# Kernel optimization log

Hardware: AMD Instinct MI355X
Metric: run time of the kernel (lower is better)

## Reference

```python
import jax, jax.numpy as jnp
import numpy as np

N_NODES = 10000
N_EDGES = 256000
H = 128   # n_hidden_feats
P = 64    # n_product_feats
NB = 8    # n_basis
NS = 10   # n_species
RH = 64   # radial MLP hidden width
RC = 5.0  # r_cutoff
AVG = 25.6  # avg_n_neighbors


def _radial(r):
    # Bessel radial basis * polynomial cutoff envelope (p = n_polynomial_cutoff = 5). r: [E,1]
    n = jnp.arange(1, NB + 1, dtype=r.dtype)
    bessel = jnp.sqrt(2.0 / RC) * jnp.sin(n * jnp.pi * r / RC) / r  # [E,NB]
    u = r / RC
    p = 5.0
    env = 1.0 - 0.5 * (p + 1) * (p + 2) * u**p + p * (p + 2) * u**(p + 1) - 0.5 * p * (p + 1) * u**(p + 2)
    env = jnp.where(u < 1.0, env, 0.0)
    return bessel * env


def _mlp(x, Ws):
    for W in Ws[:-1]:
        x = jax.nn.silu(x @ W)
    return x @ Ws[-1]


def _B0(w, A0, A1):
    # correlation-3 symmetric contractions to a scalar target; w: [N,5,P]
    dot = jnp.sum(A1 * A1, axis=-1)  # [N,P]  (rank-1 . rank-1)
    return (w[:, 0] * A0 + w[:, 1] * A0**2 + w[:, 2] * A0**3
            + w[:, 3] * dot + w[:, 4] * A0 * dot)


def _forward(positions, shifts, node_attrs,
             W_embed, Wsc1, Wup0_1, R1_0, R1_1, R1_2, R1_3,
             Wout0_1, Wout1_1, Wp0_1, Wp1_1, Wl0_1, Wl1_1,
             Wsc2, Wup0_2, Wup1_2, R2_0, R2_1, R2_2, R2_3,
             Wout0_2, Wout1_2, Wp0_2, Wl0_2,
             idx_i, idx_j):
    v = positions[idx_i] - positions[idx_j] - shifts                    # [E,3]
    r = jnp.maximum(jnp.linalg.norm(v, axis=-1, keepdims=True), 1e-9)   # [E,1]
    Y1 = v / r                                                          # Cartesian harmonics, l=1
    edge_feats = _radial(r)                                             # [E,NB]

    feats0 = node_attrs @ W_embed                                       # [N,H] scalar node embedding

    # ---- interaction 1: node feats l=0, edge attrs l<=1 -> targets l<=1 ----
    sc0 = jnp.einsum('nk,kch,nc->nh', node_attrs, Wsc1, feats0)         # per-species residual
    h0 = feats0 @ Wup0_1
    w = _mlp(edge_feats, (R1_0, R1_1, R1_2, R1_3)).reshape(-1, 2, H)    # tp weights per edge
    h0j = h0[idx_j]                                                     # [E,H]
    m0 = w[:, 0] * h0j                                                  # 0x0->0
    m1 = (w[:, 1] * h0j)[:, :, None] * Y1[:, None, :]                   # 0x1->1, [E,H,3]
    a0 = jax.ops.segment_sum(m0, idx_i, num_segments=N_NODES) / AVG
    a1 = jax.ops.segment_sum(m1, idx_i, num_segments=N_NODES) / AVG
    A0 = a0 @ Wout0_1                                                   # [N,P]
    A1 = jnp.einsum('nhd,hp->npd', a1, Wout1_1)                         # [N,P,3]

    # ---- product basis 1 (correlation 3, targets l=0 and l=1) ----
    wp0 = jnp.einsum('nk,kqp->nqp', node_attrs, Wp0_1)                  # [N,5,P]
    wp1 = jnp.einsum('nk,kqp->nqp', node_attrs, Wp1_1)                  # [N,4,P]
    B0 = _B0(wp0, A0, A1)
    dot = jnp.sum(A1 * A1, axis=-1)
    B1 = (wp1[:, 0] + wp1[:, 1] * A0 + wp1[:, 2] * A0**2 + wp1[:, 3] * dot)[:, :, None] * A1
    out0 = B0 @ Wl0_1 + sc0                                             # [N,H]
    out1 = jnp.einsum('npd,ph->nhd', B1, Wl1_1)                         # [N,H,3] (sc has no l=1 part)

    # ---- interaction 2: node feats l<=1, targets l<=1; product target l=0 ----
    sc0b = jnp.einsum('nk,kch,nc->nh', node_attrs, Wsc2, out0)
    g0 = out0 @ Wup0_2
    g1 = jnp.einsum('nhd,hg->ngd', out1, Wup1_2)
    w2 = _mlp(edge_feats, (R2_0, R2_1, R2_2, R2_3)).reshape(-1, 5, H)   # 5 tp paths
    g0j = g0[idx_j]
    g1j = g1[idx_j]
    Y1e = Y1[:, None, :]
    m0 = w2[:, 0] * g0j + w2[:, 3] * jnp.sum(g1j * Y1e, axis=-1)        # 0x0->0, 1x1->0 (dot)
    m1 = ((w2[:, 1] * g0j)[:, :, None] * Y1e                             # 0x1->1
          + w2[:, 2][:, :, None] * g1j                                   # 1x0->1
          + w2[:, 4][:, :, None] * jnp.cross(g1j, jnp.broadcast_to(Y1e, g1j.shape)))  # 1x1->1
    a0 = jax.ops.segment_sum(m0, idx_i, num_segments=N_NODES) / AVG
    a1 = jax.ops.segment_sum(m1, idx_i, num_segments=N_NODES) / AVG
    A0 = a0 @ Wout0_2
    A1 = jnp.einsum('nhd,hp->npd', a1, Wout1_2)
    wp0 = jnp.einsum('nk,kqp->nqp', node_attrs, Wp0_2)
    out0b = _B0(wp0, A0, A1) @ Wl0_2 + sc0b                             # [N,H]

    # torch returns [feats[:, :H] per layer]; the first H flattened columns are the scalar block
    return jnp.stack([out0, out0b], axis=0)                             # [2,N,H]


def setup_inputs() -> dict:
    key = jax.random.key(0)
    ks = iter(jax.random.split(key, 40))

    def nrm(shape, fan_in):
        return jax.random.normal(next(ks), shape, dtype=jnp.float32) / np.sqrt(fan_in)

    positions = jax.random.normal(next(ks), (N_NODES, 3), dtype=jnp.float32) * 8.0
    idx_i = jax.random.randint(next(ks), (N_EDGES,), 0, N_NODES)
    idx_j = jax.random.randint(next(ks), (N_EDGES,), 0, N_NODES)
    shifts = jnp.zeros((N_EDGES, 3), jnp.float32)
    species = jax.random.randint(next(ks), (N_NODES,), 0, NS)
    node_attrs = jax.nn.one_hot(species, NS, dtype=jnp.float32)

    return dict(
        positions=positions, shifts=shifts, node_attrs=node_attrs,
        W_embed=nrm((NS, H), NS),
        Wsc1=nrm((NS, H, H), H), Wup0_1=nrm((H, H), H),
        R1_0=nrm((NB, RH), NB), R1_1=nrm((RH, RH), RH), R1_2=nrm((RH, RH), RH), R1_3=nrm((RH, 2 * H), RH),
        Wout0_1=nrm((H, P), H), Wout1_1=nrm((H, P), H),
        Wp0_1=nrm((NS, 5, P), 1.0), Wp1_1=nrm((NS, 4, P), 1.0),
        Wl0_1=nrm((P, H), P), Wl1_1=nrm((P, H), P),
        Wsc2=nrm((NS, H, H), H), Wup0_2=nrm((H, H), H), Wup1_2=nrm((H, H), H),
        R2_0=nrm((NB, RH), NB), R2_1=nrm((RH, RH), RH), R2_2=nrm((RH, RH), RH), R2_3=nrm((RH, 5 * H), RH),
        Wout0_2=nrm((H, P), H), Wout1_2=nrm((H, P), H),
        Wp0_2=nrm((NS, 5, P), 1.0),
        Wl0_2=nrm((P, H), P),
        idx_i=idx_i, idx_j=idx_j,
    )


def reference(positions, shifts, node_attrs,
              W_embed, Wsc1, Wup0_1, R1_0, R1_1, R1_2, R1_3,
              Wout0_1, Wout1_1, Wp0_1, Wp1_1, Wl0_1, Wl1_1,
              Wsc2, Wup0_2, Wup1_2, R2_0, R2_1, R2_2, R2_3,
              Wout0_2, Wout1_2, Wp0_2, Wl0_2,
              idx_i, idx_j):
    return _forward(positions, shifts, node_attrs,
                    W_embed, Wsc1, Wup0_1, R1_0, R1_1, R1_2, R1_3,
                    Wout0_1, Wout1_1, Wp0_1, Wp1_1, Wl0_1, Wl1_1,
                    Wsc2, Wup0_2, Wup1_2, R2_0, R2_1, R2_2, R2_3,
                    Wout0_2, Wout1_2, Wp0_2, Wl0_2,
                    idx_i, idx_j)
```

## Files before the change

### kernel.cpp

```cpp
#include <hip/hip_runtime.h>
#include <math.h>

#define NN 10000
#define NE 256000
#define HD 128
#define PD 64
#define NBASIS 8
#define NSPEC 10
#define RHID 64
#define RCUT 5.0f
#define INV_AVG 0.0390625f
#define PI_F 3.14159265358979f
#define ECAP 12288
#define NACTCAP 8192
#define RSZ 819

__device__ __forceinline__ float silu(float x) {
    return x / (1.0f + expf(-x));
}

__global__ __launch_bounds__(256) void k_initTables(
    const float* __restrict__ na_, const float* __restrict__ We,
    const float* __restrict__ Wsc1, const float* __restrict__ Wup01,
    const float* __restrict__ Wup02, const float* __restrict__ Wsc2,
    int* __restrict__ spec, int* __restrict__ ecnt, int* cnt, int* eTot,
    int* __restrict__ scurG, int* __restrict__ actLst,
    float* __restrict__ sc0s, float* __restrict__ h0s,
    float* __restrict__ g0d, float* __restrict__ sc0bd) {
    __shared__ float ls[HD];
    int b = blockIdx.x;
    if (b < 40) {
        int n = b * 256 + threadIdx.x;
        if (n == 0) { *cnt = 0; *eTot = 0; }
        if (n < NSPEC) scurG[n] = 0;
        if (n < NACTCAP) actLst[n] = -1;
        if (n >= NN) return;
        ecnt[n] = 0;
        int s = 0;
        for (int k = 0; k < NSPEC; k++)
            if (na_[n * NSPEC + k] > 0.5f) s = k;
        spec[n] = s;
    } else {
        int s = b - 40;
        int t = threadIdx.x;
        if (t < HD) {
            float acc1 = 0.f, acc2 = 0.f;
            for (int c = 0; c < HD; c++) {
                float fe = We[s * HD + c];
                acc1 += fe * Wsc1[((size_t)s * HD + c) * HD + t];
                acc2 += fe * Wup01[c * HD + t];
            }
            sc0s[s * HD + t] = acc1;
            h0s[s * HD + t] = acc2;
            ls[t] = acc1;
        }
        __syncthreads();
        if (t < HD) {
            float a1 = 0.f, a2 = 0.f;
            for (int c = 0; c < HD; c++) {
                float v = ls[c];
                a1 += v * Wup02[c * HD + t];
                a2 += v * Wsc2[((size_t)s * HD + c) * HD + t];
            }
            g0d[s * HD + t] = a1;
            sc0bd[s * HD + t] = a2;
        }
    }
}

__global__ __launch_bounds__(256) void k_compact(
    const float* __restrict__ pos, const float* __restrict__ shifts,
    const int* __restrict__ ii, const int* __restrict__ jj,
    int* cnt, int* __restrict__ ecnt,
    int* __restrict__ ui, int* __restrict__ uj,
    float* __restrict__ uY, float* __restrict__ uF) {
    __shared__ int lTot;
    __shared__ int blockBase;
    int t = threadIdx.x;
    if (t == 0) lTot = 0;
    __syncthreads();
    int e0 = (blockIdx.x * 256 + t) * 4;
    int iv[4], jv[4], keep[4];
    float vx[4], vy[4], vz[4], rr[4];
    #pragma unroll
    for (int k = 0; k < 4; k++) {
        int e = e0 + k;
        int i = ii[e], j = jj[e];
        iv[k] = i; jv[k] = j;
        float x = pos[i * 3 + 0] - pos[j * 3 + 0] - shifts[e * 3 + 0];
        float y = pos[i * 3 + 1] - pos[j * 3 + 1] - shifts[e * 3 + 1];
        float z = pos[i * 3 + 2] - pos[j * 3 + 2] - shifts[e * 3 + 2];
        float r = sqrtf(x * x + y * y + z * z);
        r = fmaxf(r, 1e-9f);
        vx[k] = x; vy[k] = y; vz[k] = z; rr[k] = r;
        keep[k] = (r < RCUT) ? 1 : 0;
    }
    int myCnt = keep[0] + keep[1] + keep[2] + keep[3];
    int myOff = 0;
    if (myCnt) myOff = atomicAdd(&lTot, myCnt);
    __syncthreads();
    if (t == 0) blockBase = atomicAdd(cnt, lTot);
    __syncthreads();
    int slot = blockBase + myOff;
    #pragma unroll
    for (int k = 0; k < 4; k++) {
        if (!keep[k]) continue;
        int i = iv[k];
        atomicAdd(&ecnt[i], 1);
        ui[slot] = i; uj[slot] = jv[k];
        float r = rr[k];
        float inv = 1.0f / r;
        uY[slot * 3 + 0] = vx[k] * inv;
        uY[slot * 3 + 1] = vy[k] * inv;
        uY[slot * 3 + 2] = vz[k] * inv;
        float u = r * (1.0f / RCUT);
        float u5 = u * u * u * u * u;
        float env = 1.0f - 21.0f * u5 + 35.0f * u5 * u - 15.0f * u5 * u * u;
        float c0 = 0.6324555320336759f * env * inv;
        float th = PI_F * u;
        float s1, c1;
        __sincosf(th, &s1, &c1);
        float two_c1 = 2.0f * c1;
        float sp = 0.f, sn = s1;
        uF[slot * NBASIS + 0] = c0 * sn;
        #pragma unroll
        for (int b = 1; b < NBASIS; b++) {
            float s_new = two_c1 * sn - sp;
            sp = sn; sn = s_new;
            uF[slot * NBASIS + b] = c0 * sn;
        }
        slot++;
    }
}

__global__ __launch_bounds__(256) void k_assignPlace(
    const int* __restrict__ ecnt, const int* __restrict__ spec,
    int* __restrict__ ebase, int* __restrict__ ecur,
    int* eTot, int* scurG,
    int* __restrict__ actIndex, int* __restrict__ actList) {
    __shared__ int lTot;
    __shared__ int blockBase;
    __shared__ int lHist[NSPEC];
    __shared__ int lBase[NSPEC];
    int t = threadIdx.x;
    int n = blockIdx.x * 256 + t;
    if (t == 0) lTot = 0;
    if (t < NSPEC) lHist[t] = 0;
    __syncthreads();
    int ec = (n < NN) ? ecnt[n] : 0;
    int s = (n < NN) ? spec[n] : 0;
    bool act = (ec > 0);
    int myOff = 0, myIdx = 0;
    if (act) {
        myOff = atomicAdd(&lTot, ec);
        myIdx = atomicAdd(&lHist[s], 1);
    }
    __syncthreads();
    if (t == 0) blockBase = atomicAdd(eTot, lTot);
    if (t < NSPEC) lBase[t] = (lHist[t] > 0) ? atomicAdd(&scurG[t], lHist[t]) : 0;
    __syncthreads();
    if (n < NN) {
        if (act) {
            int b = blockBase + myOff;
            ebase[n] = b;
            ecur[n] = b;
            int rank = lBase[s] + myIdx;
            if (rank < RSZ) {
                int p = s * RSZ + rank;
                actList[p] = n;
                actIndex[n] = p;
            } else {
                actIndex[n] = -1;
            }
        } else {
            actIndex[n] = -1;
        }
    }
}

__global__ __launch_bounds__(256) void k_sortFill(
    const int* cnt, const int* __restrict__ ui, const int* __restrict__ uj,
    const float* __restrict__ uY, const float* __restrict__ uF,
    int* __restrict__ ecur, int* __restrict__ sj,
    float* __restrict__ sY, float* __restrict__ sF,
    const int* __restrict__ spec, const float* __restrict__ sc0s,
    const float* __restrict__ sc0bd,
    float* __restrict__ out0g, float* __restrict__ outbg) {
    int b = blockIdx.x;
    if (b < 48) {
        int e = b * 256 + threadIdx.x;
        int n = *cnt; if (n > ECAP) n = ECAP;
        if (e >= n) return;
        int slot = atomicAdd(&ecur[ui[e]], 1);
        if (slot >= ECAP) return;
        sj[slot] = uj[e];
        #pragma unroll
        for (int d = 0; d < 3; d++) sY[slot * 3 + d] = uY[e * 3 + d];
        #pragma unroll
        for (int bb = 0; bb < NBASIS; bb++) sF[slot * NBASIS + bb] = uF[e * NBASIS + bb];
    } else {
        int t = (b - 48) * 256 + threadIdx.x;
        int n = t >> 6, c = t & 63;
        if (n >= NN) return;
        int s = spec[n];
        out0g[(size_t)n * HD + c] = sc0s[s * HD + c];
        out0g[(size_t)n * HD + 64 + c] = sc0s[s * HD + 64 + c];
        outbg[(size_t)n * HD + c] = sc0bd[s * HD + c];
        outbg[(size_t)n * HD + 64 + c] = sc0bd[s * HD + 64 + c];
    }
}

__global__ __launch_bounds__(256) void k_hid(
    const int* cnt, const float* __restrict__ sF,
    const float* __restrict__ A0, const float* __restrict__ A1, const float* __restrict__ A2,
    const float* __restrict__ B0, const float* __restrict__ B1, const float* __restrict__ B2,
    float* __restrict__ xh1, float* __restrict__ xh2) {
    __shared__ float sf[64 * 9];
    __shared__ float xA[64 * 65];
    __shared__ float xB[64 * 65];
    int t = threadIdx.x;
    int ne = *cnt; if (ne > ECAP) ne = ECAP;
    int eBase = blockIdx.x * 64;
    if (eBase >= ne) return;
    const float* W0 = (blockIdx.y == 0) ? A0 : B0;
    const float* W1 = (blockIdx.y == 0) ? A1 : B1;
    const float* W2 = (blockIdx.y == 0) ? A2 : B2;
    float* dst = (blockIdx.y == 0) ? xh1 : xh2;
    if (t < 128) {
        float4 v = *(const float4*)(sF + (size_t)eBase * NBASIS + t * 4);
        int e = t >> 1, c = (t & 1) * 4;
        float* d = &sf[e * 9 + c];
        d[0] = v.x; d[1] = v.y; d[2] = v.z; d[3] = v.w;
    }
    __syncthreads();
    int sgrp = t >> 4;
    int cg = (t & 15) * 4;
    {
        float acc[4][4] = {};
        #pragma unroll
        for (int c = 0; c < NBASIS; c++) {
            float xk[4];
            #pragma unroll
            for (int k = 0; k < 4; k++) xk[k] = sf[(sgrp * 4 + k) * 9 + c];
            float4 wv = *(const float4*)(W0 + c * RHID + cg);
            float wq[4] = {wv.x, wv.y, wv.z, wv.w};
            #pragma unroll
            for (int k = 0; k < 4; k++)
                #pragma unroll
                for (int q = 0; q < 4; q++)
                    acc[k][q] += xk[k] * wq[q];
        }
        #pragma unroll
        for (int k = 0; k < 4; k++)
            #pragma unroll
            for (int q = 0; q < 4; q++)
                xA[(sgrp * 4 + k) * 65 + cg + q] = silu(acc[k][q]);
    }
    __syncthreads();
    {
        float acc[4][4] = {};
        for (int c = 0; c < RHID; c++) {
            float xk[4];
            #pragma unroll
            for (int k = 0; k < 4; k++) xk[k] = xA[(sgrp * 4 + k) * 65 + c];
            float4 wv = *(const float4*)(W1 + c * RHID + cg);
            float wq[4] = {wv.x, wv.y, wv.z, wv.w};
            #pragma unroll
            for (int k = 0; k < 4; k++)
                #pragma unroll
                for (int q = 0; q < 4; q++)
                    acc[k][q] += xk[k] * wq[q];
        }
        #pragma unroll
        for (int k = 0; k < 4; k++)
            #pragma unroll
            for (int q = 0; q < 4; q++)
                xB[(sgrp * 4 + k) * 65 + cg + q] = silu(acc[k][q]);
    }
    __syncthreads();
    {
        float acc[4][4] = {};
        for (int c = 0; c < RHID; c++) {
            float xk[4];
            #pragma unroll
            for (int k = 0; k < 4; k++) xk[k] = xB[(sgrp * 4 + k) * 65 + c];
            float4 wv = *(const float4*)(W2 + c * RHID + cg);
            float wq[4] = {wv.x, wv.y, wv.z, wv.w};
            #pragma unroll
            for (int k = 0; k < 4; k++)
                #pragma unroll
                for (int q = 0; q < 4; q++)
                    acc[k][q] += xk[k] * wq[q];
        }
        #pragma unroll
        for (int k = 0; k < 4; k++) {
            int e = eBase + sgrp * 4 + k;
            if (e < ne) {
                *(float4*)(dst + (size_t)e * RHID + cg) =
                    make_float4(silu(acc[k][0]), silu(acc[k][1]),
                                silu(acc[k][2]), silu(acc[k][3]));
            }
        }
    }
}

__global__ __launch_bounds__(256) void k_wmat(
    const int* cnt, const float* __restrict__ xh1, const float* __restrict__ xh2,
    const float* __restrict__ A3, const float* __restrict__ B3,
    float* __restrict__ ew1, float* __restrict__ ew2) {
    __shared__ float sX[64 * 65];
    int t = threadIdx.x;
    int ne = *cnt; if (ne > ECAP) ne = ECAP;
    int y = blockIdx.y;
    int eBase = blockIdx.x * 64;
    if (eBase >= ne) return;
    const float* X; const float* W; float* dst; int ncol, col0;
    if (y < 2) { X = xh1; W = A3; dst = ew1; ncol = 2 * HD; col0 = y * 128; }
    else       { X = xh2; W = B3; dst = ew2; ncol = 5 * HD; col0 = (y - 2) * 128; }
    {
        const float4* src = (const float4*)(X + (size_t)eBase * RHID);
        #pragma unroll
        for (int it = 0; it < 4; it++) {
            int idx = t + it * 256;
            float4 v = src[idx];
            int e = idx >> 4, c4 = (idx & 15) * 4;
            float* d = &sX[e * 65 + c4];
            d[0] = v.x; d[1] = v.y; d[2] = v.z; d[3] = v.w;
        }
    }
    __syncthreads();
    int sgrp = t >> 4;
    int cg = col0 + (t & 15) * 8;
    float acc[4][8] = {};
    for (int c = 0; c < RHID; c++) {
        float xk[4];
        #pragma unroll
        for (int k = 0; k < 4; k++) xk[k] = sX[(sgrp * 4 + k) * 65 + c];
        float4 wA = *(const float4*)(W + (size_t)c * ncol + cg);
        float4 wB = *(const float4*)(W + (size_t)c * ncol + cg + 4);
        float wv[8] = {wA.x, wA.y, wA.z, wA.w, wB.x, wB.y, wB.z, wB.w};
        #pragma unroll
        for (int k = 0; k < 4; k++)
            #pragma unroll
            for (int q = 0; q < 8; q++)
                acc[k][q] += xk[k] * wv[q];
    }
    #pragma unroll
    for (int k = 0; k < 4; k++) {
        int e = eBase + sgrp * 4 + k;
        *(float4*)(dst + (size_t)e * ncol + cg) =
            make_float4(acc[k][0], acc[k][1], acc[k][2], acc[k][3]);
        *(float4*)(dst + (size_t)e * ncol + cg + 4) =
            make_float4(acc[k][4], acc[k][5], acc[k][6], acc[k][7]);
    }
}

__global__ __launch_bounds__(256) void k_agg1(
    const int* __restrict__ actList,
    const int* __restrict__ ebase, const int* __restrict__ ecnt,
    const int* __restrict__ sj, const float* __restrict__ sY,
    const float* __restrict__ ew, const int* __restrict__ spec,
    const float* __restrict__ h0s, float* __restrict__ a0c, float* __restrict__ a1c) {
    int lane = threadIdx.x & 63;
    int ia = (blockIdx.x * 256 + threadIdx.x) >> 6;
    int h = blockIdx.y * 64;
    int n = actList[ia];
    if (n < 0) return;
    int eb = ebase[n], ec = ecnt[n];
    float a0 = 0.f;
    float a1[3] = {0,0,0};
    for (int idx = eb; idx < eb + ec; idx++) {
        int j = sj[idx];
        int sp = spec[j];
        float h0 = h0s[sp * HD + h + lane];
        const float* w = ew + (size_t)idx * 256;
        float w0 = w[h + lane], w1 = w[128 + h + lane];
        a0 += w0 * h0;
        float m1 = w1 * h0;
        #pragma unroll
        for (int d = 0; d < 3; d++) a1[d] += m1 * sY[idx * 3 + d];
    }
    a0c[(size_t)ia * HD + h + lane] = a0 * INV_AVG;
    #pragma unroll
    for (int d = 0; d < 3; d++)
        a1c[((size_t)d * NACTCAP + ia) * HD + h + lane] = a1[d] * INV_AVG;
}

__global__ __launch_bounds__(256) void k_proj(
    const int* __restrict__ actList,
    const float* __restrict__ x0buf, const float* __restrict__ x1buf,
    const float* __restrict__ W0, const float* __restrict__ W1,
    float* __restrict__ am0, float* __restrict__ am1) {
    __shared__ float sX[16 * HD];
    int lane = threadIdx.x & 63;
    int w = __builtin_amdgcn_readfirstlane((int)(threadIdx.x >> 6));
    int y = blockIdx.y;
    const float* X = (y == 0) ? x0buf : (x1buf + (size_t)(y - 1) * NACTCAP * HD);
    const float* W = (y == 0) ? W0 : W1;
    int iaBase = blockIdx.x * 16;
    {
        const float4* src = (const float4*)(X + (size_t)iaBase * HD);
        float4* d4 = (float4*)sX;
        #pragma unroll
        for (int it = 0; it < 2; it++)
            d4[threadIdx.x + it * 256] = src[threadIdx.x + it * 256];
    }
    __syncthreads();
    bool any = false;
    int ia0 = iaBase + w * 4;
    #pragma unroll
    for (int k = 0; k < 4; k++) any = any || (actList[ia0 + k] >= 0);
    if (!any) return;
    float* dst = (y == 0) ? am0 : (am1 + (size_t)(y - 1) * NACTCAP * PD);
    int w4 = w * 4;
    float acc[4] = {0,0,0,0};
    for (int c = 0; c < HD; c += 4) {
        float4 xv[4];
        #pragma unroll
        for (int k = 0; k < 4; k++) xv[k] = *(const float4*)&sX[(w4 + k) * HD + c];
        #pragma unroll
        for (int cc = 0; cc < 4; cc++) {
            float wv = W[(c + cc) * PD + lane];
            #pragma unroll
            for (int k = 0; k < 4; k++) {
                float xc = (cc==0)?xv[k].x:(cc==1)?xv[k].y:(cc==2)?xv[k].z:xv[k].w;
                acc[k] += xc * wv;
            }
        }
    }
    #pragma unroll
    for (int k = 0; k < 4; k++) dst[(size_t)(ia0 + k) * PD + lane] = acc[k];
}

__global__ __launch_bounds__(256) void k_bout(
    const int* __restrict__ actList,
    const float* __restrict__ am0, const float* __restrict__ am1,
    const int* __restrict__ spec,
    const float* __restrict__ Wp0, const float* __restrict__ Wp1,
    const float* __restrict__ Wl0, const float* __restrict__ Wl1,
    const float* __restrict__ sc0s,
    float* __restrict__ out0g, float* __restrict__ out0c, float* __restrict__ out1c) {
    __shared__ float sB[4][8][PD];
    int lane = threadIdx.x & 63;
    int w = __builtin_amdgcn_readfirstlane((int)(threadIdx.x >> 6));
    int y = blockIdx.y;
    int bs = y >> 1, h = (y & 1) * 64;
    int ia0 = (blockIdx.x * 4 + w) * 8;
    int nv[8], sk[8];
    bool any = false;
    #pragma unroll
    for (int k = 0; k < 8; k++) {
        nv[k] = actList[ia0 + k];
        any = any || (nv[k] >= 0);
        sk[k] = spec[(nv[k] >= 0) ? nv[k] : 0];
    }
    if (!any) return;
    #pragma unroll
    for (int k = 0; k < 8; k++) {
        int ia = ia0 + k;
        int s = sk[k];
        float A0v = am0[(size_t)ia * PD + lane];
        float a1x = am1[((size_t)0 * NACTCAP + ia) * PD + lane];
        float a1y = am1[((size_t)1 * NACTCAP + ia) * PD + lane];
        float a1z = am1[((size_t)2 * NACTCAP + ia) * PD + lane];
        float dot = a1x * a1x + a1y * a1y + a1z * a1z;
        float A02 = A0v * A0v;
        float B;
        if (bs == 0) {
            const float* wp = Wp0 + (size_t)(s * 5) * PD;
            B = wp[lane] * A0v + wp[PD + lane] * A02 + wp[2 * PD + lane] * A02 * A0v +
                wp[3 * PD + lane] * dot + wp[4 * PD + lane] * A0v * dot;
        } else {
            const float* wp = Wp1 + (size_t)(s * 4) * PD;
            float fac = wp[lane] + wp[PD + lane] * A0v + wp[2 * PD + lane] * A02 + wp[3 * PD + lane] * dot;
            float a1d = (bs == 1) ? a1x : ((bs == 2) ? a1y : a1z);
            B = fac * a1d;
        }
        sB[w][k][lane] = B;
    }
    const float* Wl = (bs == 0) ? Wl0 : Wl1;
    float o[8] = {0,0,0,0,0,0,0,0};
    for (int q = 0; q < PD; q += 4) {
        float4 bq[8];
        #pragma unroll
        for (int k = 0; k < 8; k++) bq[k] = *(const float4*)&sB[w][k][q];
        #pragma unroll
        for (int qq = 0; qq < 4; qq++) {
            float wl = Wl[(q + qq) * HD + h + lane];
            #pragma unroll
            for (int k = 0; k < 8; k++) {
                float b = (qq==0)?bq[k].x:(qq==1)?bq[k].y:(qq==2)?bq[k].z:bq[k].w;
                o[k] += b * wl;
            }
        }
    }
    if (bs == 0) {
        #pragma unroll
        for (int k = 0; k < 8; k++) {
            int ia = ia0 + k;
            float v = o[k] + sc0s[sk[k] * HD + h + lane];
            if (nv[k] >= 0) out0g[(size_t)nv[k] * HD + h + lane] = v;
            out0c[(size_t)ia * HD + h + lane] = v;
        }
    } else {
        float* dst = out1c + (size_t)(bs - 1) * NACTCAP * HD;
        #pragma unroll
        for (int k = 0; k < 8; k++)
            dst[(size_t)(ia0 + k) * HD + h + lane] = o[k];
    }
}

__global__ __launch_bounds__(256) void k_g(
    const int* __restrict__ actList, const int* __restrict__ spec,
    const float* __restrict__ out0c, const float* __restrict__ out1c,
    const float* __restrict__ Wsc2, const float* __restrict__ Wup02, const float* __restrict__ Wup12,
    float* __restrict__ sc0bc, float* __restrict__ g0c, float* __restrict__ g1c) {
    __shared__ float sX[64 * 129];
    __shared__ int sSpec[64];
    __shared__ int sB0, sAny, sMis;
    int t = threadIdx.x;
    int st = blockIdx.y;
    int slotBase = blockIdx.x * 64;
    const float* X = (st <= 1) ? out0c : (out1c + (size_t)(st - 2) * NACTCAP * HD);
    if (t < 64) {
        int n = actList[slotBase + t];
        sSpec[t] = (n >= 0) ? spec[n] : -1;
    }
    __syncthreads();
    if (t == 0) {
        int sb = 0, any = 0, mis = 0;
        for (int k = 0; k < 64; k++) {
            int sv = sSpec[k];
            if (sv >= 0) {
                if (!any) { sb = sv; any = 1; }
                else if (sv != sb) mis = 1;
            }
        }
        sB0 = sb; sAny = any; sMis = mis;
    }
    __syncthreads();
    if (!sAny) return;
    {
        const float4* src = (const float4*)(X + (size_t)slotBase * HD);
        #pragma unroll
        for (int it = 0; it < 8; it++) {
            int idx = t + it * 256;
            float4 v = src[idx];
            int e = idx >> 5, c4 = (idx & 31) * 4;
            float* d = &sX[e * 129 + c4];
            d[0] = v.x; d[1] = v.y; d[2] = v.z; d[3] = v.w;
        }
    }
    __syncthreads();
    const float* Wt = (st == 0) ? (Wsc2 + (size_t)sB0 * HD * HD)
                    : ((st == 1) ? Wup02 : Wup12);
    float* dst = (st == 0) ? sc0bc : ((st == 1) ? g0c : (g1c + (size_t)(st - 2) * NACTCAP * HD));
    int sgrp = t >> 4;
    int cg = (t & 15) * 8;
    float acc[4][8] = {};
    for (int c = 0; c < HD; c++) {
        float xk[4];
        #pragma unroll
        for (int k = 0; k < 4; k++) xk[k] = sX[(sgrp * 4 + k) * 129 + c];
        float4 wA = *(const float4*)(Wt + (size_t)c * HD + cg);
        float4 wB = *(const float4*)(Wt + (size_t)c * HD + cg + 4);
        float wv[8] = {wA.x, wA.y, wA.z, wA.w, wB.x, wB.y, wB.z, wB.w};
        #pragma unroll
        for (int k = 0; k < 4; k++)
            #pragma unroll
            for (int q = 0; q < 8; q++)
                acc[k][q] += xk[k] * wv[q];
    }
    #pragma unroll
    for (int k = 0; k < 4; k++) {
        int slot = slotBase + sgrp * 4 + k;
        *(float4*)(dst + (size_t)slot * HD + cg) =
            make_float4(acc[k][0], acc[k][1], acc[k][2], acc[k][3]);
        *(float4*)(dst + (size_t)slot * HD + cg + 4) =
            make_float4(acc[k][4], acc[k][5], acc[k][6], acc[k][7]);
    }
    if (st == 0 && sMis) {
        __syncthreads();
        for (int k = 0; k < 64; k++) {
            int sv = sSpec[k];
            if (sv < 0 || sv == sB0) continue;
            if (t < HD) {
                const float* Wm = Wsc2 + (size_t)sv * HD * HD;
                float p = 0.f;
                for (int c = 0; c < HD; c++) p += sX[k * 129 + c] * Wm[c * HD + t];
                sc0bc[(size_t)(slotBase + k) * HD + t] = p;
            }
        }
    }
}

__global__ __launch_bounds__(256) void k_agg2(
    const int* __restrict__ actList,
    const int* __restrict__ ebase, const int* __restrict__ ecnt,
    const int* __restrict__ sj, const float* __restrict__ sY,
    const float* __restrict__ ew, const int* __restrict__ spec,
    const int* __restrict__ actIndex,
    const float* __restrict__ g0c, const float* __restrict__ g1c,
    const float* __restrict__ g0d,
    float* __restrict__ a0c, float* __restrict__ a1c) {
    int lane = threadIdx.x & 63;
    int ia = (blockIdx.x * 256 + threadIdx.x) >> 6;
    int h = blockIdx.y * 64;
    int n = actList[ia];
    if (n < 0) return;
    int eb = ebase[n], ec = ecnt[n];
    float m0 = 0.f;
    float s1[3] = {0,0,0};
    for (int idx = eb; idx < eb + ec; idx++) {
        int j = sj[idx];
        float Yx = sY[idx * 3 + 0], Yy = sY[idx * 3 + 1], Yz = sY[idx * 3 + 2];
        int ji = actIndex[j];
        float gv, gx, gy, gz;
        if (ji >= 0) {
            gv = g0c[(size_t)ji * HD + h + lane];
            gx = g1c[((size_t)0 * NACTCAP + ji) * HD + h + lane];
            gy = g1c[((size_t)1 * NACTCAP + ji) * HD + h + lane];
            gz = g1c[((size_t)2 * NACTCAP + ji) * HD + h + lane];
        } else {
            gv = g0d[spec[j] * HD + h + lane];
            gx = gy = gz = 0.f;
        }
        const float* wr = ew + (size_t)idx * 640;
        float w0 = wr[h + lane];
        float w1 = wr[128 + h + lane];
        float w2 = wr[256 + h + lane];
        float w3 = wr[384 + h + lane];
        float w4 = wr[512 + h + lane];
        float dot = gx * Yx + gy * Yy + gz * Yz;
        m0 += w0 * gv + w3 * dot;
        float cx = gy * Yz - gz * Yy, cy = gz * Yx - gx * Yz, cz = gx * Yy - gy * Yx;
        s1[0] += w1 * gv * Yx + w2 * gx + w4 * cx;
        s1[1] += w1 * gv * Yy + w2 * gy + w4 * cy;
        s1[2] += w1 * gv * Yz + w2 * gz + w4 * cz;
    }
    a0c[(size_t)ia * HD + h + lane] = m0 * INV_AVG;
    #pragma unroll
    for (int d = 0; d < 3; d++)
        a1c[((size_t)d * NACTCAP + ia) * HD + h + lane] = s1[d] * INV_AVG;
}

__global__ __launch_bounds__(256) void k_outC(
    const int* __restrict__ actList, const int* __restrict__ spec,
    const float* __restrict__ am0, const float* __restrict__ am1,
    const float* __restrict__ Wp0, const float* __restrict__ Wl0,
    const float* __restrict__ sc0bc, float* __restrict__ outbg) {
    __shared__ float sB[4][8][PD];
    int lane = threadIdx.x & 63;
    int w = __builtin_amdgcn_readfirstlane((int)(threadIdx.x >> 6));
    int h = blockIdx.y * 64;
    int ia0 = (blockIdx.x * 4 + w) * 8;
    int nv[8];
    bool any = false;
    #pragma unroll
    for (int k = 0; k < 8; k++) { nv[k] = actList[ia0 + k]; any = any || (nv[k] >= 0); }
    if (!any) return;
    #pragma unroll
    for (int k = 0; k < 8; k++) {
        int ia = ia0 + k;
        int s = spec[(nv[k] >= 0) ? nv[k] : 0];
        float A0v = am0[(size_t)ia * PD + lane];
        float a1x = am1[((size_t)0 * NACTCAP + ia) * PD + lane];
        float a1y = am1[((size_t)1 * NACTCAP + ia) * PD + lane];
        float a1z = am1[((size_t)2 * NACTCAP + ia) * PD + lane];
        float dot = a1x * a1x + a1y * a1y + a1z * a1z;
        float A02 = A0v * A0v;
        const float* wp = Wp0 + (size_t)(s * 5) * PD;
        sB[w][k][lane] = wp[lane] * A0v + wp[PD + lane] * A02 + wp[2 * PD + lane] * A02 * A0v +
                         wp[3 * PD + lane] * dot + wp[4 * PD + lane] * A0v * dot;
    }
    float o[8] = {0,0,0,0,0,0,0,0};
    for (int q = 0; q < PD; q += 4) {
        float4 bq[8];
        #pragma unroll
        for (int k = 0; k < 8; k++) bq[k] = *(const float4*)&sB[w][k][q];
        #pragma unroll
        for (int qq = 0; qq < 4; qq++) {
            float wl = Wl0[(q + qq) * HD + h + lane];
            #pragma unroll
            for (int k = 0; k < 8; k++) {
                float b = (qq==0)?bq[k].x:(qq==1)?bq[k].y:(qq==2)?bq[k].z:bq[k].w;
                o[k] += b * wl;
            }
        }
    }
    #pragma unroll
    for (int k = 0; k < 8; k++) {
        if (nv[k] < 0) continue;
        int ia = ia0 + k;
        outbg[(size_t)nv[k] * HD + h + lane] = o[k] + sc0bc[(size_t)ia * HD + h + lane];
    }
}

extern "C" void kernel_launch(void* const* d_in, const int* in_sizes, int n_in,
                              void* d_out, int out_size, void* d_ws, size_t ws_size,
                              hipStream_t stream) {
    const float* pos    = (const float*)d_in[0];
    const float* shifts = (const float*)d_in[1];
    const float* na     = (const float*)d_in[2];
    const float* We     = (const float*)d_in[3];
    const float* Wsc1   = (const float*)d_in[4];
    const float* Wup01  = (const float*)d_in[5];
    const float* R10    = (const float*)d_in[6];
    const float* R11    = (const float*)d_in[7];
    const float* R12    = (const float*)d_in[8];
    const float* R13    = (const float*)d_in[9];
    const float* Wout01 = (const float*)d_in[10];
    const float* Wout11 = (const float*)d_in[11];
    const float* Wp01   = (const float*)d_in[12];
    const float* Wp11   = (const float*)d_in[13];
    const float* Wl01   = (const float*)d_in[14];
    const float* Wl11   = (const float*)d_in[15];
    const float* Wsc2   = (const float*)d_in[16];
    const float* Wup02  = (const float*)d_in[17];
    const float* Wup12  = (const float*)d_in[18];
    const float* R20    = (const float*)d_in[19];
    const float* R21    = (const float*)d_in[20];
    const float* R22    = (const float*)d_in[21];
    const float* R23    = (const float*)d_in[22];
    const float* Wout02 = (const float*)d_in[23];
    const float* Wout12 = (const float*)d_in[24];
    const float* Wp02   = (const float*)d_in[25];
    const float* Wl02   = (const float*)d_in[26];
    const int*   idx_i  = (const int*)d_in[27];
    const int*   idx_j  = (const int*)d_in[28];
    float* out = (float*)d_out;
    float* outb = out + (size_t)NN * HD;

    char* ws = (char*)d_ws;
    size_t off = 0;
    auto alloc = [&](size_t bytes) -> char* {
        char* pp = ws + off;
        off += (bytes + 255) & ~(size_t)255;
        return pp;
    };
    int*   cnt    = (int*)alloc(4);
    int*   eTot   = (int*)alloc(4);
    int*   scurG  = (int*)alloc(NSPEC * 4);
    int*   spec   = (int*)alloc((size_t)NN * 4);
    int*   ecnt   = (int*)alloc((size_t)NN * 4);
    int*   ebase  = (int*)alloc((size_t)NN * 4);
    int*   ecur   = (int*)alloc((size_t)NN * 4);
    int*   actIdx = (int*)alloc((size_t)NN * 4);
    int*   actLst = (int*)alloc((size_t)NACTCAP * 4);
    float* sc0s   = (float*)alloc((size_t)NSPEC * HD * 4);
    float* h0s    = (float*)alloc((size_t)NSPEC * HD * 4);
    float* g0d    = (float*)alloc((size_t)NSPEC * HD * 4);
    float* sc0bd  = (float*)alloc((size_t)NSPEC * HD * 4);
    int*   sj     = (int*)alloc((size_t)ECAP * 4);
    float* sYv    = (float*)alloc((size_t)ECAP * 3 * 4);
    float* sFv    = (float*)alloc((size_t)ECAP * NBASIS * 4);
    float* xh1    = (float*)alloc((size_t)ECAP * RHID * 4);
    float* xh2    = (float*)alloc((size_t)ECAP * RHID * 4);
    float* ew1    = (float*)alloc((size_t)ECAP * 256 * 4);
    float* ew2    = (float*)alloc((size_t)ECAP * 640 * 4);
    int*   ui     = (int*)ew2;
    int*   uj     = ui + NE;
    float* uY     = (float*)(uj + NE);
    float* uF     = uY + (size_t)NE * 3;
    float* a0c    = (float*)alloc((size_t)NACTCAP * HD * 4);
    float* a1c    = (float*)alloc((size_t)NACTCAP * HD * 3 * 4);
    float* am0    = (float*)alloc((size_t)NACTCAP * PD * 4);
    float* am1    = (float*)alloc((size_t)NACTCAP * PD * 3 * 4);
    float* out0c  = (float*)alloc((size_t)NACTCAP * HD * 4);
    float* out1c  = (float*)alloc((size_t)NACTCAP * HD * 3 * 4);
    float* g0c    = (float*)alloc((size_t)NACTCAP * HD * 4);
    float* g1c    = (float*)alloc((size_t)NACTCAP * HD * 3 * 4);
    float* sc0bc  = (float*)alloc((size_t)NACTCAP * HD * 4);

    k_initTables<<<50, 256, 0, stream>>>(na, We, Wsc1, Wup01, Wup02, Wsc2,
                                         spec, ecnt, cnt, eTot, scurG, actLst,
                                         sc0s, h0s, g0d, sc0bd);
    k_compact<<<NE / 1024, 256, 0, stream>>>(pos, shifts, idx_i, idx_j, cnt, ecnt,
                                             ui, uj, uY, uF);
    k_assignPlace<<<(NN + 255) / 256, 256, 0, stream>>>(ecnt, spec, ebase, ecur,
                                                        eTot, scurG, actIdx, actLst);
    k_sortFill<<<48 + (NN * 64) / 256, 256, 0, stream>>>(cnt, ui, uj, uY, uF, ecur,
                                                         sj, sYv, sFv,
                                                         spec, sc0s, sc0bd, out, outb);
    k_hid<<<dim3(ECAP / 64, 2), 256, 0, stream>>>(cnt, sFv, R10, R11, R12,
                                                  R20, R21, R22, xh1, xh2);
    k_wmat<<<dim3(ECAP / 64, 7), 256, 0, stream>>>(cnt, xh1, xh2, R13, R23, ew1, ew2);
    k_agg1<<<dim3(NACTCAP / 4, 2), 256, 0, stream>>>(actLst, ebase, ecnt, sj, sYv, ew1,
                                                     spec, h0s, a0c, a1c);
    k_proj<<<dim3(NACTCAP / 16, 4), 256, 0, stream>>>(actLst, a0c, a1c, Wout01, Wout11,
                                                      am0, am1);
    k_bout<<<dim3(NACTCAP / 32, 8), 256, 0, stream>>>(actLst, am0, am1, spec,
                                                      Wp01, Wp11, Wl01, Wl11, sc0s,
                                                      out, out0c, out1c);
    k_g<<<dim3(NACTCAP / 64, 5), 256, 0, stream>>>(actLst, spec, out0c, out1c,
                                                   Wsc2, Wup02, Wup12, sc0bc, g0c, g1c);
    k_agg2<<<dim3(NACTCAP / 4, 2), 256, 0, stream>>>(actLst, ebase, ecnt, sj, sYv, ew2,
                                                     spec, actIdx, g0c, g1c, g0d, a0c, a1c);
    k_proj<<<dim3(NACTCAP / 16, 4), 256, 0, stream>>>(actLst, a0c, a1c, Wout02, Wout12,
                                                      am0, am1);
    k_outC<<<dim3(NACTCAP / 32, 2), 256, 0, stream>>>(actLst, spec, am0, am1, Wp02, Wl02,
                                                      sc0bc, outb);
}
```

Before: 172.6 us.

## Fuse final projection and output contraction into one tiled kernel

Replaces the last k_proj and k_outC launches with a single kernel. Each block stages 64 active nodes' aggregated features in shared memory, computes the Wout projections into registers, and evaluates the symmetric contraction into shared memory. It then does the Wl0 output matmul with a register tile. This drops one launch and the am0/am1 round trip through global memory. In exchange the grid is much smaller (128 blocks, no y-split), which lowers parallelism, and shared-memory use rises.

```diff
diff --git a/kernel.cpp b/kernel.cpp
--- a/kernel.cpp
+++ b/kernel.cpp
@@ -644,55 +644,110 @@
         a1c[((size_t)d * NACTCAP + ia) * HD + h + lane] = s1[d] * INV_AVG;
 }
 
-__global__ __launch_bounds__(256) void k_outC(
+__global__ __launch_bounds__(256) void k_projOutC(
     const int* __restrict__ actList, const int* __restrict__ spec,
-    const float* __restrict__ am0, const float* __restrict__ am1,
+    const float* __restrict__ a0c, const float* __restrict__ a1c,
+    const float* __restrict__ W0, const float* __restrict__ W1,
     const float* __restrict__ Wp0, const float* __restrict__ Wl0,
     const float* __restrict__ sc0bc, float* __restrict__ outbg) {
-    __shared__ float sB[4][8][PD];
-    int lane = threadIdx.x & 63;
-    int w = __builtin_amdgcn_readfirstlane((int)(threadIdx.x >> 6));
-    int h = blockIdx.y * 64;
-    int ia0 = (blockIdx.x * 4 + w) * 8;
-    int nv[8];
-    bool any = false;
-    #pragma unroll
-    for (int k = 0; k < 8; k++) { nv[k] = actList[ia0 + k]; any = any || (nv[k] >= 0); }
-    if (!any) return;
-    #pragma unroll
-    for (int k = 0; k < 8; k++) {
-        int ia = ia0 + k;
-        int s = spec[(nv[k] >= 0) ? nv[k] : 0];
-        float A0v = am0[(size_t)ia * PD + lane];
-        float a1x = am1[((size_t)0 * NACTCAP + ia) * PD + lane];
-        float a1y = am1[((size_t)1 * NACTCAP + ia) * PD + lane];
-        float a1z = am1[((size_t)2 * NACTCAP + ia) * PD + lane];
-        float dot = a1x * a1x + a1y * a1y + a1z * a1z;
-        float A02 = A0v * A0v;
+    __shared__ float sX[64 * 129];
+    __shared__ float sB[64 * 65];
+    __shared__ int sSpec[64];
+    __shared__ int sNv[64];
+    int t = threadIdx.x;
+    int slotBase = blockIdx.x * 64;
+    if (t < 64) {
+        int n = actList[slotBase + t];
+        sNv[t] = n;
+        sSpec[t] = (n >= 0) ? spec[n] : 0;
+    }
+    __syncthreads();
+    bool anyAct = false;
+    for (int k = 0; k < 64; k++) anyAct = anyAct || (sNv[k] >= 0);
+    if (!anyAct) return;
+    int sgrp = t >> 4;
+    int c4 = (t & 15) * 4;
+    float am[4][4][4];
+    #pragma unroll 1
+    for (int st = 0; st < 4; st++) {
+        const float* X = (st == 0) ? a0c : (a1c + (size_t)(st - 1) * NACTCAP * HD);
+        const float* W = (st == 0) ? W0 : W1;
+        __syncthreads();
+        {
+            const float4* src = (const float4*)(X + (size_t)slotBase * HD);
+            #pragma unroll
+            for (int it = 0; it < 8; it++) {
+                int idx = t + it * 256;
+                float4 v = src[idx];
+                int e = idx >> 5, cc = (idx & 31) * 4;
+                float* d = &sX[e * 129 + cc];
+                d[0] = v.x; d[1] = v.y; d[2] = v.z; d[3] = v.w;
+            }
+        }
+        __syncthreads();
+        float acc[4][4] = {};
+        for (int c = 0; c < HD; c++) {
+            float xk[4];
+            #pragma unroll
+            for (int k = 0; k < 4; k++) xk[k] = sX[(sgrp * 4 + k) * 129 + c];
+            float4 wv = *(const float4*)(W + (size_t)c * PD + c4);
+            float wq[4] = {wv.x, wv.y, wv.z, wv.w};
+            #pragma unroll
+            for (int k = 0; k < 4; k++)
+                #pragma unroll
+                for (int q = 0; q < 4; q++)
+                    acc[k][q] += xk[k] * wq[q];
+        }
+        #pragma unroll
+        for (int k = 0; k < 4; k++)
+            #pragma unroll
+            for (int q = 0; q < 4; q++)
+                am[st][k][q] = acc[k][q];
+    }
+    __syncthreads();
+    #pragma unroll
+    for (int k = 0; k < 4; k++) {
+        int slot = sgrp * 4 + k;
+        int s = sSpec[slot];
         const float* wp = Wp0 + (size_t)(s * 5) * PD;
-        sB[w][k][lane] = wp[lane] * A0v + wp[PD + lane] * A02 + wp[2 * PD + lane] * A02 * A0v +
-                         wp[3 * PD + lane] * dot + wp[4 * PD + lane] * A0v * dot;
-    }
-    float o[8] = {0,0,0,0,0,0,0,0};
-    for (int q = 0; q < PD; q += 4) {
-        float4 bq[8];
-        #pragma unroll
-        for (int k = 0; k < 8; k++) bq[k] = *(const float4*)&sB[w][k][q];
-        #pragma unroll
-        for (int qq = 0; qq < 4; qq++) {
-            float wl = Wl0[(q + qq) * HD + h + lane];
-            #pragma unroll
-            for (int k = 0; k < 8; k++) {
-                float b = (qq==0)?bq[k].x:(qq==1)?bq[k].y:(qq==2)?bq[k].z:bq[k].w;
-                o[k] += b * wl;
-            }
-        }
-    }
-    #pragma unroll
-    for (int k = 0; k < 8; k++) {
-        if (nv[k] < 0) continue;
-        int ia = ia0 + k;
-        outbg[(size_t)nv[k] * HD + h + lane] = o[k] + sc0bc[(size_t)ia * HD + h + lane];
+        #pragma unroll
+        for (int q = 0; q < 4; q++) {
+            int p = c4 + q;
+            float A0v = am[0][k][q];
+            float a1x = am[1][k][q], a1y = am[2][k][q], a1z = am[3][k][q];
+            float dot = a1x * a1x + a1y * a1y + a1z * a1z;
+            float A02 = A0v * A0v;
+            sB[slot * 65 + p] = wp[p] * A0v + wp[PD + p] * A02 +
+                                wp[2 * PD + p] * A02 * A0v +
+                                wp[3 * PD + p] * dot + wp[4 * PD + p] * A0v * dot;
+        }
+    }
+    __syncthreads();
+    int cg = (t & 15) * 8;
+    float o[4][8] = {};
+    for (int q = 0; q < PD; q++) {
+        float bk[4];
+        #pragma unroll
+        for (int k = 0; k < 4; k++) bk[k] = sB[(sgrp * 4 + k) * 65 + q];
+        float4 wA = *(const float4*)(Wl0 + (size_t)q * HD + cg);
+        float4 wB = *(const float4*)(Wl0 + (size_t)q * HD + cg + 4);
+        float wv[8] = {wA.x, wA.y, wA.z, wA.w, wB.x, wB.y, wB.z, wB.w};
+        #pragma unroll
+        for (int k = 0; k < 4; k++)
+            #pragma unroll
+            for (int qq = 0; qq < 8; qq++)
+                o[k][qq] += bk[k] * wv[qq];
+    }
+    #pragma unroll
+    for (int k = 0; k < 4; k++) {
+        int slot = sgrp * 4 + k;
+        int n = sNv[slot];
+        if (n < 0) continue;
+        size_t sbase = (size_t)(slotBase + slot) * HD + cg;
+        size_t obase = (size_t)n * HD + cg;
+        #pragma unroll
+        for (int qq = 0; qq < 8; qq++)
+            outbg[obase + qq] = o[k][qq] + sc0bc[sbase + qq];
     }
 }
 
@@ -796,8 +851,6 @@
                                                    Wsc2, Wup02, Wup12, sc0bc, g0c, g1c);
     k_agg2<<<dim3(NACTCAP / 4, 2), 256, 0, stream>>>(actLst, ebase, ecnt, sj, sYv, ew2,
                                                      spec, actIdx, g0c, g1c, g0d, a0c, a1c);
-    k_proj<<<dim3(NACTCAP / 16, 4), 256, 0, stream>>>(actLst, a0c, a1c, Wout02, Wout12,
-                                                      am0, am1);
-    k_outC<<<dim3(NACTCAP / 32, 2), 256, 0, stream>>>(actLst, spec, am0, am1, Wp02, Wl02,
-                                                      sc0bc, outb);
-}
+    k_projOutC<<<NACTCAP / 64, 256, 0, stream>>>(actLst, spec, a0c, a1c, Wout02, Wout12,
+                                                 Wp02, Wl02, sc0bc, outb);
+}
```

After: 196.2 us. 13.7% more time.
